# Performance work log

Measured on AMD Instinct MI355X. Metric: run time of the kernel, lower is better.

Reference implementation:

```python
import jax, jax.numpy as jnp
import numpy as np

B, S, D = 4, 4096, 2048

def setup_inputs() -> dict:
    key = jax.random.key(0)
    k1, k2 = jax.random.split(key)
    k = jax.random.normal(k1, (B, S, D), dtype=jnp.float32)
    v = jax.random.normal(k2, (B, S, D), dtype=jnp.float32)
    kv_state = jnp.zeros((D, D), dtype=jnp.float32)
    k_sum = jnp.zeros((D,), dtype=jnp.float32)
    return {"k": k, "v": v, "kv_state": kv_state, "k_sum": k_sum}

def reference(k, v, kv_state, k_sum):
    b, s, d = k.shape
    k_flat = k.reshape(-1, d)  # (N, D), N = B*S
    v_flat = v.reshape(-1, d)
    # Accumulate outer-product state: kv_state += sum_i k_i v_i^T
    kv_new = kv_state + jnp.einsum('nd,ne->de', k_flat, v_flat)
    ks_new = k_sum + k_flat.sum(axis=0)
    # Readout: context = k @ kv_state^T ; normalizer = k @ k_sum
    context = jnp.einsum('nd,ed->ne', k_flat, kv_new).reshape(b, s, d)
    normalizer = (k_flat @ ks_new).reshape(b, s, 1)
    return context, normalizer
```

## Files before the change

kernel.cpp:

```cpp
#include <hip/hip_runtime.h>
#include <hip/hip_bf16.h>
#include <cstdio>
#include <cstdint>

#define NBIG 16384
#define DDIM 2048
#define SPLITK 4

#define BM 256
#define BN 256
#define BKT 64

typedef __attribute__((ext_vector_type(4))) float f32x4;
typedef __attribute__((ext_vector_type(8))) short bf16x8;

__device__ __forceinline__ unsigned short f2bf(float f) {
  union { float f; unsigned u; } v; v.f = f;
  return (unsigned short)((v.u + 0x7FFFu + ((v.u >> 16) & 1u)) >> 16);
}

__device__ __forceinline__ void gll16(const void* g, void* l) {
  auto gp = reinterpret_cast<const __attribute__((address_space(1))) unsigned int*>(
      reinterpret_cast<uintptr_t>(g));
  auto lp = reinterpret_cast<__attribute__((address_space(3))) unsigned int*>(
      (unsigned int)reinterpret_cast<uintptr_t>(l));
  __builtin_amdgcn_global_load_lds(gp, lp, 16, 0, 0);
}

__device__ __forceinline__ void waitvm8() { asm volatile("s_waitcnt vmcnt(8)" ::: "memory"); }
__device__ __forceinline__ void waitvm0() { asm volatile("s_waitcnt vmcnt(0)" ::: "memory"); }
__device__ __forceinline__ void barrier_pinned() {
  __builtin_amdgcn_sched_barrier(0);
  __builtin_amdgcn_s_barrier();
  __builtin_amdgcn_sched_barrier(0);
}

__global__ __launch_bounds__(256) void prep_kernel(
    const float* __restrict__ k, const float* __restrict__ v,
    unsigned short* __restrict__ KT, unsigned short* __restrict__ VT,
    unsigned short* __restrict__ Kbf, float* __restrict__ ks)
{
  __shared__ unsigned short sm[64][66];
  __shared__ float sks[64];
  const int t = threadIdx.x;
  const int tiles_d = DDIM / 64;
  const int n0 = (blockIdx.x / tiles_d) * 64;
  const int d0 = (blockIdx.x % tiles_d) * 64;
  const bool is_k = (blockIdx.y == 0);
  const float* __restrict__ src = is_k ? k : v;
  unsigned short* __restrict__ dstT = is_k ? KT : VT;

  const int r = t >> 4;
  const int c = (t & 15) * 4;

  if (t < 64) sks[t] = 0.f;
  __syncthreads();

  float a0 = 0.f, a1 = 0.f, a2 = 0.f, a3 = 0.f;
#pragma unroll
  for (int i = 0; i < 4; ++i) {
    const int row = i * 16 + r;
    f32x4 val = *reinterpret_cast<const f32x4*>(&src[(size_t)(n0 + row) * DDIM + d0 + c]);
    unsigned short b0 = f2bf(val.x), b1 = f2bf(val.y), b2 = f2bf(val.z), b3 = f2bf(val.w);
    sm[row][c + 0] = b0; sm[row][c + 1] = b1;
    sm[row][c + 2] = b2; sm[row][c + 3] = b3;
    if (is_k) {
      unsigned int p0 = (unsigned)b0 | ((unsigned)b1 << 16);
      unsigned int p1 = (unsigned)b2 | ((unsigned)b3 << 16);
      *reinterpret_cast<uint2*>(&Kbf[(size_t)(n0 + row) * DDIM + d0 + c]) = make_uint2(p0, p1);
      a0 += val.x; a1 += val.y; a2 += val.z; a3 += val.w;
    }
  }
  if (is_k) {
    atomicAdd(&sks[c + 0], a0);
    atomicAdd(&sks[c + 1], a1);
    atomicAdd(&sks[c + 2], a2);
    atomicAdd(&sks[c + 3], a3);
  }
  __syncthreads();

#pragma unroll
  for (int i = 0; i < 4; ++i) {
    const int rowp = i * 16 + r;
    unsigned int p0 = (unsigned)sm[c + 0][rowp] | ((unsigned)sm[c + 1][rowp] << 16);
    unsigned int p1 = (unsigned)sm[c + 2][rowp] | ((unsigned)sm[c + 3][rowp] << 16);
    *reinterpret_cast<uint2*>(&dstT[(size_t)(d0 + rowp) * NBIG + n0 + c]) = make_uint2(p0, p1);
  }
  if (is_k && t < 64) atomicAdd(&ks[d0 + t], sks[t]);
}

__global__ void init_ks_kernel(const float* __restrict__ ksum, float* __restrict__ ks) {
  int i = blockIdx.x * 256 + threadIdx.x;
  if (i < DDIM) ks[i] = ksum[i];
}

__global__ __launch_bounds__(512, 2) void gemm256_kernel(
    const unsigned short* __restrict__ A, const unsigned short* __restrict__ B,
    float* __restrict__ C, int lda, int ldb, int kchunk, long long zstride)
{
  __shared__ unsigned short Abuf[2][BM * BKT];
  __shared__ unsigned short Bbuf[2][BN * BKT];

  const int t = threadIdx.x, lane = t & 63, w = t >> 6;
  const int wm = w >> 2, wn = w & 3;
  const int m0 = blockIdx.y * BM, n0 = blockIdx.x * BN;
  const int kbeg = blockIdx.z * kchunk;
  const int NT = kchunk / BKT;

  const int srow = lane >> 3;
  const int sgr  = (lane & 7) ^ srow;
  const unsigned short* Ag = A + (size_t)(m0 + srow) * lda + kbeg + sgr * 8;
  const unsigned short* Bg = B + (size_t)(n0 + srow) * ldb + kbeg + sgr * 8;

  const int hi = lane >> 4;
  const int lo7 = lane & 7;
  const int swz0 = ((0 + hi) ^ lo7) * 8;
  const int swz1 = ((4 + hi) ^ lo7) * 8;
  const int arow = (wm * 128 + (lane & 15)) * BKT;
  const int brow = (wn * 64 + (lane & 15)) * BKT;

  auto stage_op = [&](const unsigned short* G, unsigned short* Lbase, int ld_,
                      int kt, int half) {
    const unsigned short* g = G + (size_t)(half * 128 + w * 16) * ld_ + (size_t)kt * BKT;
    unsigned short* l = Lbase + (half * 128 + w * 16) * BKT;
    gll16(g, l);
    gll16(g + (size_t)8 * ld_, l + 8 * BKT);
  };

  stage_op(Bg, Bbuf[0], ldb, 0, 0); stage_op(Bg, Bbuf[0], ldb, 0, 1);
  stage_op(Ag, Abuf[0], lda, 0, 0); stage_op(Ag, Abuf[0], lda, 0, 1);
  stage_op(Bg, Bbuf[1], ldb, 1, 0); stage_op(Bg, Bbuf[1], ldb, 1, 1);
  stage_op(Ag, Abuf[1], lda, 1, 0); stage_op(Ag, Abuf[1], lda, 1, 1);
  waitvm8();
  __builtin_amdgcn_s_barrier();
  __builtin_amdgcn_sched_barrier(0);

  f32x4 acc[8][4] = {};

#pragma unroll 2
  for (int tl = 0; tl < NT; ++tl) {
    const int q = tl & 1;
    const unsigned short* Al = Abuf[q];
    const unsigned short* Bl = Bbuf[q];
    bf16x8 af[4][2], bA[2][2], bB[2][2];

#pragma unroll
    for (int m = 0; m < 4; ++m) {
      af[m][0] = *reinterpret_cast<const bf16x8*>(Al + arow + m * 16 * BKT + swz0);
      af[m][1] = *reinterpret_cast<const bf16x8*>(Al + arow + m * 16 * BKT + swz1);
    }
#pragma unroll
    for (int n = 0; n < 2; ++n) {
      bA[n][0] = *reinterpret_cast<const bf16x8*>(Bl + brow + n * 16 * BKT + swz0);
      bA[n][1] = *reinterpret_cast<const bf16x8*>(Bl + brow + n * 16 * BKT + swz1);
    }
    __builtin_amdgcn_s_setprio(1);
#pragma unroll
    for (int m = 0; m < 4; ++m)
#pragma unroll
      for (int n = 0; n < 2; ++n) {
        acc[m][n] = __builtin_amdgcn_mfma_f32_16x16x32_bf16(af[m][0], bA[n][0], acc[m][n], 0, 0, 0);
        acc[m][n] = __builtin_amdgcn_mfma_f32_16x16x32_bf16(af[m][1], bA[n][1], acc[m][n], 0, 0, 0);
      }
    __builtin_amdgcn_s_setprio(0);

#pragma unroll
    for (int n = 0; n < 2; ++n) {
      bB[n][0] = *reinterpret_cast<const bf16x8*>(Bl + brow + (32 + n * 16) * BKT + swz0);
      bB[n][1] = *reinterpret_cast<const bf16x8*>(Bl + brow + (32 + n * 16) * BKT + swz1);
    }
    __builtin_amdgcn_s_setprio(1);
#pragma unroll
    for (int m = 0; m < 4; ++m)
#pragma unroll
      for (int n = 0; n < 2; ++n) {
        acc[m][2 + n] = __builtin_amdgcn_mfma_f32_16x16x32_bf16(af[m][0], bB[n][0], acc[m][2 + n], 0, 0, 0);
        acc[m][2 + n] = __builtin_amdgcn_mfma_f32_16x16x32_bf16(af[m][1], bB[n][1], acc[m][2 + n], 0, 0, 0);
      }
    __builtin_amdgcn_s_setprio(0);
    barrier_pinned();

    if (tl + 2 < NT) {
      stage_op(Bg, Bbuf[q], ldb, tl + 2, 0);
      stage_op(Bg, Bbuf[q], ldb, tl + 2, 1);
    }
#pragma unroll
    for (int m = 0; m < 4; ++m) {
      af[m][0] = *reinterpret_cast<const bf16x8*>(Al + arow + (64 + m * 16) * BKT + swz0);
      af[m][1] = *reinterpret_cast<const bf16x8*>(Al + arow + (64 + m * 16) * BKT + swz1);
    }
    __builtin_amdgcn_s_setprio(1);
#pragma unroll
    for (int m = 0; m < 4; ++m)
#pragma unroll
      for (int n = 0; n < 2; ++n) {
        acc[4 + m][n] = __builtin_amdgcn_mfma_f32_16x16x32_bf16(af[m][0], bA[n][0], acc[4 + m][n], 0, 0, 0);
        acc[4 + m][n] = __builtin_amdgcn_mfma_f32_16x16x32_bf16(af[m][1], bA[n][1], acc[4 + m][n], 0, 0, 0);
      }
    __builtin_amdgcn_s_setprio(0);
    barrier_pinned();

    if (tl + 2 < NT) {
      stage_op(Ag, Abuf[q], lda, tl + 2, 0);
      stage_op(Ag, Abuf[q], lda, tl + 2, 1);
    }
    __builtin_amdgcn_s_setprio(1);
#pragma unroll
    for (int m = 0; m < 4; ++m)
#pragma unroll
      for (int n = 0; n < 2; ++n) {
        acc[4 + m][2 + n] = __builtin_amdgcn_mfma_f32_16x16x32_bf16(af[m][0], bB[n][0], acc[4 + m][2 + n], 0, 0, 0);
        acc[4 + m][2 + n] = __builtin_amdgcn_mfma_f32_16x16x32_bf16(af[m][1], bB[n][1], acc[4 + m][2 + n], 0, 0, 0);
      }
    __builtin_amdgcn_s_setprio(0);
    if (tl + 1 < NT) {
      if (tl + 2 < NT) waitvm8();
      else             waitvm0();
      __builtin_amdgcn_s_barrier();
      __builtin_amdgcn_sched_barrier(0);
    }
  }

  float* Cz = C + (size_t)blockIdx.z * zstride;
  const int crow0 = m0 + wm * 128 + hi * 4;
  const int ccol0 = n0 + wn * 64 + (lane & 15);
#pragma unroll
  for (int m = 0; m < 8; ++m)
#pragma unroll
    for (int n = 0; n < 4; ++n)
#pragma unroll
      for (int j = 0; j < 4; ++j)
        Cz[(size_t)(crow0 + m * 16 + j) * DDIM + ccol0 + n * 16] = acc[m][n][j];
}

__global__ __launch_bounds__(256) void kvconv_kernel(
    const float* __restrict__ kvp, const float* __restrict__ kvst,
    unsigned short* __restrict__ kvbf)
{
  size_t i = ((size_t)blockIdx.x * 256 + threadIdx.x) * 4;
  f32x4 s = *reinterpret_cast<const f32x4*>(&kvst[i]);
#pragma unroll
  for (int z = 0; z < SPLITK; ++z) {
    f32x4 p = *reinterpret_cast<const f32x4*>(&kvp[(size_t)z * DDIM * DDIM + i]);
    s.x += p.x; s.y += p.y; s.z += p.z; s.w += p.w;
  }
  unsigned int p0 = (unsigned)f2bf(s.x) | ((unsigned)f2bf(s.y) << 16);
  unsigned int p1 = (unsigned)f2bf(s.z) | ((unsigned)f2bf(s.w) << 16);
  *reinterpret_cast<uint2*>(&kvbf[i]) = make_uint2(p0, p1);
}

__global__ __launch_bounds__(256) void norm_kernel(
    const float* __restrict__ k, const float* __restrict__ ks, float* __restrict__ out)
{
  const int lane = threadIdx.x & 63;
  const int w = threadIdx.x >> 6;
  const int row = blockIdx.x * 4 + w;
  const float* kr = k + (size_t)row * DDIM;
  float s = 0.f;
#pragma unroll
  for (int i = 0; i < DDIM / 256; ++i) {
    f32x4 a = *reinterpret_cast<const f32x4*>(&kr[i * 256 + lane * 4]);
    f32x4 b = *reinterpret_cast<const f32x4*>(&ks[i * 256 + lane * 4]);
    s += a.x * b.x + a.y * b.y + a.z * b.z + a.w * b.w;
  }
  for (int off = 32; off; off >>= 1) s += __shfl_down(s, off, 64);
  if (lane == 0) out[row] = s;
}

extern "C" void kernel_launch(void* const* d_in, const int* in_sizes, int n_in,
                              void* d_out, int out_size, void* d_ws, size_t ws_size,
                              hipStream_t stream) {
  const float* k    = (const float*)d_in[0];
  const float* v    = (const float*)d_in[1];
  const float* kvst = (const float*)d_in[2];
  const float* ksum = (const float*)d_in[3];

  const size_t SZ_T = (size_t)DDIM * NBIG * 2;
  const size_t WS_NEED = SZ_T * 3 + (size_t)DDIM * DDIM * 2 + DDIM * 4;
  if (ws_size < WS_NEED) {
    fprintf(stderr, "kernel_launch: ws too small %zu < %zu\n", ws_size, WS_NEED);
    return;
  }
  char* ws = (char*)d_ws;
  unsigned short* KT   = (unsigned short*)ws;
  unsigned short* VT   = (unsigned short*)(ws + SZ_T);
  unsigned short* Kbf  = (unsigned short*)(ws + 2 * SZ_T);
  unsigned short* KVbf = (unsigned short*)(ws + 3 * SZ_T);
  float* ks            = (float*)(ws + 3 * SZ_T + (size_t)DDIM * DDIM * 2);

  float* ctx = (float*)d_out;
  float* nrm = ctx + (size_t)NBIG * DDIM;
  float* kvp = ctx;

  init_ks_kernel<<<(DDIM + 255) / 256, 256, 0, stream>>>(ksum, ks);
  prep_kernel<<<dim3((NBIG / 64) * (DDIM / 64), 2), 256, 0, stream>>>(k, v, KT, VT, Kbf, ks);
  gemm256_kernel<<<dim3(DDIM / BN, DDIM / BM, SPLITK), 512, 0, stream>>>(
      KT, VT, kvp, NBIG, NBIG, NBIG / SPLITK, (long long)DDIM * DDIM);
  kvconv_kernel<<<(DDIM * DDIM) / (256 * 4), 256, 0, stream>>>(kvp, kvst, KVbf);
  gemm256_kernel<<<dim3(DDIM / BN, NBIG / BM, 1), 512, 0, stream>>>(
      Kbf, KVbf, ctx, DDIM, DDIM, DDIM, 0);
  norm_kernel<<<NBIG / 4, 256, 0, stream>>>(k, ks, nrm);
}
```

Measured before the change: 403.5 us.

## Add XCD-aware block swizzle and ping-pong barrier phases to bf16 GEMM loop

Remaps workgroup IDs so consecutive tiles are placed on the same XCD, which is meant to improve L2 reuse of shared A/B panels. The main loop is restructured into explicit phases: LDS fragment loads, then a barrier and lgkmcnt wait, then an MFMA cluster. The second A fragment set moves into separate registers (af2) so it can be loaded before the B prefetch is issued. The aim is ping-pong style scheduling between the two waves sharing each SIMD, but the extra barriers and registers may cost occupancy or add sync stalls.

```diff
diff --git a/kernel.cpp b/kernel.cpp
--- a/kernel.cpp
+++ b/kernel.cpp
@@ -29,10 +29,17 @@
 
 __device__ __forceinline__ void waitvm8() { asm volatile("s_waitcnt vmcnt(8)" ::: "memory"); }
 __device__ __forceinline__ void waitvm0() { asm volatile("s_waitcnt vmcnt(0)" ::: "memory"); }
-__device__ __forceinline__ void barrier_pinned() {
-  __builtin_amdgcn_sched_barrier(0);
-  __builtin_amdgcn_s_barrier();
-  __builtin_amdgcn_sched_barrier(0);
+#define SB0 __builtin_amdgcn_sched_barrier(0)
+
+__device__ __forceinline__ void xcd_swizzle(int& bx, int& by, int& bz) {
+  const unsigned nx = gridDim.x, ny = gridDim.y;
+  const unsigned nwg = nx * ny * gridDim.z;
+  unsigned wg = blockIdx.x + nx * (blockIdx.y + ny * blockIdx.z);
+  wg = (wg & 7u) * (nwg >> 3) + (wg >> 3);
+  bx = wg % nx;
+  unsigned r = wg / nx;
+  by = r % ny;
+  bz = r / ny;
 }
 
 __global__ __launch_bounds__(256) void prep_kernel(
@@ -101,10 +108,13 @@
   __shared__ unsigned short Abuf[2][BM * BKT];
   __shared__ unsigned short Bbuf[2][BN * BKT];
 
+  int bx, by, bz;
+  xcd_swizzle(bx, by, bz);
+
   const int t = threadIdx.x, lane = t & 63, w = t >> 6;
   const int wm = w >> 2, wn = w & 3;
-  const int m0 = blockIdx.y * BM, n0 = blockIdx.x * BN;
-  const int kbeg = blockIdx.z * kchunk;
+  const int m0 = by * BM, n0 = bx * BN;
+  const int kbeg = bz * kchunk;
   const int NT = kchunk / BKT;
 
   const int srow = lane >> 3;
@@ -133,7 +143,7 @@
   stage_op(Ag, Abuf[1], lda, 1, 0); stage_op(Ag, Abuf[1], lda, 1, 1);
   waitvm8();
   __builtin_amdgcn_s_barrier();
-  __builtin_amdgcn_sched_barrier(0);
+  SB0;
 
   f32x4 acc[8][4] = {};
 
@@ -142,7 +152,8 @@
     const int q = tl & 1;
     const unsigned short* Al = Abuf[q];
     const unsigned short* Bl = Bbuf[q];
-    bf16x8 af[4][2], bA[2][2], bB[2][2];
+    const bool pf = (tl + 2 < NT);
+    bf16x8 af[4][2], af2[4][2], bA[2][2], bB[2][2];
 
 #pragma unroll
     for (int m = 0; m < 4; ++m) {
@@ -154,6 +165,9 @@
       bA[n][0] = *reinterpret_cast<const bf16x8*>(Bl + brow + n * 16 * BKT + swz0);
       bA[n][1] = *reinterpret_cast<const bf16x8*>(Bl + brow + n * 16 * BKT + swz1);
     }
+    SB0; __builtin_amdgcn_s_barrier();
+    asm volatile("s_waitcnt lgkmcnt(0)" ::: "memory");
+    SB0;
     __builtin_amdgcn_s_setprio(1);
 #pragma unroll
     for (int m = 0; m < 4; ++m)
@@ -163,12 +177,16 @@
         acc[m][n] = __builtin_amdgcn_mfma_f32_16x16x32_bf16(af[m][1], bA[n][1], acc[m][n], 0, 0, 0);
       }
     __builtin_amdgcn_s_setprio(0);
+    SB0; __builtin_amdgcn_s_barrier(); SB0;
 
 #pragma unroll
     for (int n = 0; n < 2; ++n) {
       bB[n][0] = *reinterpret_cast<const bf16x8*>(Bl + brow + (32 + n * 16) * BKT + swz0);
       bB[n][1] = *reinterpret_cast<const bf16x8*>(Bl + brow + (32 + n * 16) * BKT + swz1);
     }
+    SB0; __builtin_amdgcn_s_barrier();
+    asm volatile("s_waitcnt lgkmcnt(0)" ::: "memory");
+    SB0;
     __builtin_amdgcn_s_setprio(1);
 #pragma unroll
     for (int m = 0; m < 4; ++m)
@@ -178,50 +196,55 @@
         acc[m][2 + n] = __builtin_amdgcn_mfma_f32_16x16x32_bf16(af[m][1], bB[n][1], acc[m][2 + n], 0, 0, 0);
       }
     __builtin_amdgcn_s_setprio(0);
-    barrier_pinned();
-
-    if (tl + 2 < NT) {
+    SB0; __builtin_amdgcn_s_barrier(); SB0;
+
+#pragma unroll
+    for (int m = 0; m < 4; ++m) {
+      af2[m][0] = *reinterpret_cast<const bf16x8*>(Al + arow + (64 + m * 16) * BKT + swz0);
+      af2[m][1] = *reinterpret_cast<const bf16x8*>(Al + arow + (64 + m * 16) * BKT + swz1);
+    }
+    if (pf) {
       stage_op(Bg, Bbuf[q], ldb, tl + 2, 0);
       stage_op(Bg, Bbuf[q], ldb, tl + 2, 1);
     }
-#pragma unroll
-    for (int m = 0; m < 4; ++m) {
-      af[m][0] = *reinterpret_cast<const bf16x8*>(Al + arow + (64 + m * 16) * BKT + swz0);
-      af[m][1] = *reinterpret_cast<const bf16x8*>(Al + arow + (64 + m * 16) * BKT + swz1);
-    }
+    SB0; __builtin_amdgcn_s_barrier();
+    asm volatile("s_waitcnt lgkmcnt(0)" ::: "memory");
+    SB0;
     __builtin_amdgcn_s_setprio(1);
 #pragma unroll
     for (int m = 0; m < 4; ++m)
 #pragma unroll
       for (int n = 0; n < 2; ++n) {
-        acc[4 + m][n] = __builtin_amdgcn_mfma_f32_16x16x32_bf16(af[m][0], bA[n][0], acc[4 + m][n], 0, 0, 0);
-        acc[4 + m][n] = __builtin_amdgcn_mfma_f32_16x16x32_bf16(af[m][1], bA[n][1], acc[4 + m][n], 0, 0, 0);
+        acc[4 + m][n] = __builtin_amdgcn_mfma_f32_16x16x32_bf16(af2[m][0], bA[n][0], acc[4 + m][n], 0, 0, 0);
+        acc[4 + m][n] = __builtin_amdgcn_mfma_f32_16x16x32_bf16(af2[m][1], bA[n][1], acc[4 + m][n], 0, 0, 0);
       }
     __builtin_amdgcn_s_setprio(0);
-    barrier_pinned();
-
-    if (tl + 2 < NT) {
+    SB0; __builtin_amdgcn_s_barrier(); SB0;
+
+    if (pf) {
       stage_op(Ag, Abuf[q], lda, tl + 2, 0);
       stage_op(Ag, Abuf[q], lda, tl + 2, 1);
     }
+    SB0; __builtin_amdgcn_s_barrier(); SB0;
     __builtin_amdgcn_s_setprio(1);
 #pragma unroll
     for (int m = 0; m < 4; ++m)
 #pragma unroll
       for (int n = 0; n < 2; ++n) {
-        acc[4 + m][2 + n] = __builtin_amdgcn_mfma_f32_16x16x32_bf16(af[m][0], bB[n][0], acc[4 + m][2 + n], 0, 0, 0);
-        acc[4 + m][2 + n] = __builtin_amdgcn_mfma_f32_16x16x32_bf16(af[m][1], bB[n][1], acc[4 + m][2 + n], 0, 0, 0);
+        acc[4 + m][2 + n] = __builtin_amdgcn_mfma_f32_16x16x32_bf16(af2[m][0], bB[n][0], acc[4 + m][2 + n], 0, 0, 0);
+        acc[4 + m][2 + n] = __builtin_amdgcn_mfma_f32_16x16x32_bf16(af2[m][1], bB[n][1], acc[4 + m][2 + n], 0, 0, 0);
       }
     __builtin_amdgcn_s_setprio(0);
+    SB0;
     if (tl + 1 < NT) {
-      if (tl + 2 < NT) waitvm8();
-      else             waitvm0();
+      if (pf) waitvm8();
+      else    waitvm0();
       __builtin_amdgcn_s_barrier();
-      __builtin_amdgcn_sched_barrier(0);
-    }
-  }
-
-  float* Cz = C + (size_t)blockIdx.z * zstride;
+      SB0;
+    }
+  }
+
+  float* Cz = C + (size_t)bz * zstride;
   const int crow0 = m0 + wm * 128 + hi * 4;
   const int ccol0 = n0 + wn * 64 + (lane & 15);
 #pragma unroll
```

Measured after the change: 413.9 us. +2.6%, slower.
